# Optimization experiments

Measured on AMD Instinct MI355X. Metric: run time of the kernel, lower is better.

## Reference

```python
import jax, jax.numpy as jnp
import numpy as np

Q, M, B, D, H, DH, DI = 512, 512, 8, 1024, 16, 64, 4096
K = Q + M  # klen = rlen


def layer_norm(x, g, b, eps=1e-5):
    mu = x.mean(-1, keepdims=True)
    var = ((x - mu) ** 2).mean(-1, keepdims=True)
    return (x - mu) / jnp.sqrt(var + eps) * g + b


def rel_shift(x):
    # x: [qlen, klen, bsz, n_heads] -> Transformer-XL relative shift
    q, k = x.shape[0], x.shape[1]
    zero_pad = jnp.zeros((q, 1) + x.shape[2:], x.dtype)
    x_padded = jnp.concatenate([zero_pad, x], axis=1)          # [q, k+1, b, n]
    x_padded = x_padded.reshape((k + 1, q) + x.shape[2:])       # row-major reinterpret
    return x_padded[1:].reshape(x.shape)


def setup_inputs() -> dict:
    key = jax.random.key(0)
    ks = jax.random.split(key, 12)
    rn = lambda k, s: jax.random.normal(k, s, jnp.float32)
    # causal mask with memory: query i (absolute pos i+M) cannot attend to key j > i+M
    i = jnp.arange(Q)[:, None]
    j = jnp.arange(K)[None, :]
    attn_mask = (j > (i + M))[:, :, None]  # [Q, K, 1] bool
    return dict(
        w=rn(ks[0], (Q, B, D)),
        r=rn(ks[1], (K, D)),
        r_w_bias=rn(ks[2], (H, DH)) * 0.02,
        r_r_bias=rn(ks[3], (H, DH)) * 0.02,
        mems=rn(ks[4], (M, B, D)),
        attn_mask=attn_mask,
        Wqkv=rn(ks[5], (3 * H * DH, D)) * 0.02,
        Wr=rn(ks[6], (H * DH, D)) * 0.02,
        Wo=rn(ks[7], (D, H * DH)) * 0.02,
        ln1_g=jnp.ones(D), ln1_b=jnp.zeros(D),
        W1=rn(ks[8], (DI, D)) * 0.02, b1=jnp.zeros(DI),
        W2=rn(ks[9], (D, DI)) * 0.02, b2=jnp.zeros(D),
        ln2_g=jnp.ones(D), ln2_b=jnp.zeros(D),
    )


def reference(w, r, r_w_bias, r_r_bias, mems, attn_mask,
              Wqkv, Wr, Wo, ln1_g, ln1_b, W1, b1, W2, b2, ln2_g, ln2_b):
    qlen, bsz = w.shape[0], w.shape[1]
    scale = 1.0 / (DH ** 0.5)

    cat = jnp.concatenate([mems, w], axis=0)                 # [K, B, D]
    heads = cat @ Wqkv.T                                     # [K, B, 3*H*DH] (post-lnorm: no LN here)
    q, k, v = jnp.split(heads, 3, axis=-1)
    q = q[-qlen:]                                            # [Q, B, H*DH]
    r_k = r @ Wr.T                                           # [K, H*DH]

    klen = k.shape[0]
    q = q.reshape(qlen, bsz, H, DH)
    k = k.reshape(klen, bsz, H, DH)
    v = v.reshape(klen, bsz, H, DH)
    r_k = r_k.reshape(klen, H, DH)

    AC = jnp.einsum('ibnd,jbnd->ijbn', q + r_w_bias, k)      # content score
    BD = rel_shift(jnp.einsum('ibnd,jnd->ijbn', q + r_r_bias, r_k))  # position score
    attn_score = (AC + BD) * scale                           # [Q, K, B, H]
    attn_score = jnp.where(attn_mask[:, :, :, None], -jnp.inf, attn_score)

    attn_prob = jax.nn.softmax(attn_score, axis=1)
    attn_vec = jnp.einsum('ijbn,jbnd->ibnd', attn_prob, v)
    attn_vec = attn_vec.reshape(qlen, bsz, H * DH)
    attn_out = attn_vec @ Wo.T
    out1 = layer_norm(w + attn_out, ln1_g, ln1_b)            # post-lnorm residual

    ff = jax.nn.relu(out1 @ W1.T + b1) @ W2.T + b2           # position-wise FFN
    out = layer_norm(out1 + ff, ln2_g, ln2_b)
    return out
```

## Files before the change

kernel.cpp:

```cpp
#include <hip/hip_runtime.h>
#include <hip/hip_bf16.h>

typedef __hip_bfloat16 bf16;

typedef __attribute__((ext_vector_type(8))) short frag8;
typedef __attribute__((ext_vector_type(4))) float f32x4;

__device__ __forceinline__ bf16 f2bf(float f) { return __float2bfloat16(f); }

__device__ __forceinline__ float u16f(unsigned short u) {
  union { unsigned int i; float f; } c; c.i = ((unsigned int)u) << 16; return c.f;
}
__device__ __forceinline__ unsigned short bfbits(float f) {
  union { bf16 b; unsigned short u; } c; c.b = __float2bfloat16(f); return c.u;
}
__device__ __forceinline__ float tof(float x) { return x; }
__device__ __forceinline__ float tof(bf16 x)  { return __bfloat162float(x); }

__device__ __forceinline__ void gload_lds16(const bf16* g, short* l) {
  __builtin_amdgcn_global_load_lds(
      (const __attribute__((address_space(1))) void*)g,
      (__attribute__((address_space(3))) void*)l, 16, 0, 0);
}

template<int CTRL>
__device__ __forceinline__ float dppmax(float x) {
  return fmaxf(x, __int_as_float(__builtin_amdgcn_update_dpp(
      0, __float_as_int(x), CTRL, 0xF, 0xF, true)));
}
__device__ __forceinline__ float rowmax16(float x) {
  x = dppmax<0x128>(x);
  x = dppmax<0x124>(x);
  x = dppmax<0x4E>(x);
  x = dppmax<0xB1>(x);
  return x;
}
template<int CTRL>
__device__ __forceinline__ float dppadd(float x) {
  return x + __int_as_float(__builtin_amdgcn_update_dpp(
      0, __float_as_int(x), CTRL, 0xF, 0xF, true));
}
__device__ __forceinline__ float rowsum16(float x) {
  x = dppadd<0x128>(x);
  x = dppadd<0x124>(x);
  x = dppadd<0x4E>(x);
  x = dppadd<0xB1>(x);
  return x;
}

#define EP_PLAIN 0
#define EP_RK    2
#define EP_Q     3
#define EP_KV    4

struct CvtArgs {
  const float* src[8];
  bf16* dst[8];
  int cum[9];
};
__global__ __launch_bounds__(256)
void cvt8(CvtArgs a)
{
  const int i = blockIdx.x * 256 + threadIdx.x;
  if (i >= a.cum[8]) return;
  int seg = 7;
  #pragma unroll
  for (int s2 = 6; s2 >= 0; --s2) if (i < a.cum[s2 + 1]) seg = s2;
  const int o = i - a.cum[seg];
  float4 v = ((const float4*)a.src[seg])[o];
  ushort4 u;
  u.x = bfbits(v.x); u.y = bfbits(v.y); u.z = bfbits(v.z); u.w = bfbits(v.w);
  ((ushort4*)a.dst[seg])[o] = u;
}

template<typename TRES, int BKT>
__global__ __launch_bounds__(256)
void mgemm(const bf16* __restrict__ A, const bf16* __restrict__ W,
           const float* __restrict__ bias, const TRES* __restrict__ res,
           bf16* __restrict__ out,
           bf16* __restrict__ qwb, bf16* __restrict__ qrb,
           bf16* __restrict__ kbo, bf16* __restrict__ vto,
           const float* __restrict__ rwbias, const float* __restrict__ rrbias,
           int M, int N, int K, int mode, int relu, int gn, int CM, int CN)
{
  __shared__ __align__(16) short sAm[2][128 * BKT];
  __shared__ __align__(16) short sBm[2][128 * BKT];
  const int tid  = threadIdx.x;
  const int lane = tid & 63;
  const int wave = tid >> 6;
  const int quad = lane >> 4;
  const int l15  = lane & 15;
  const int xcd = blockIdx.x & 7;
  const int k_  = blockIdx.x >> 3;
  const int ncx = gn / CN;
  const int chy = xcd / ncx;
  const int chx = xcd - chy * ncx;
  const int m0 = (chy * CM + k_ / CN) * 128;
  const int n0 = (chx * CN + (k_ % CN)) * 128;
  const int wm = (wave >> 1) * 64;
  const int wn = (wave & 1) * 64;

  const int lr = tid >> 2;
  const int lc = (tid & 3) << 3;

  const bf16* aptr0 = A + (size_t)(m0 + lr) * K + lc;
  const bf16* aptr1 = aptr0 + (size_t)64 * K;
  const bf16* wptr0 = W + (size_t)(n0 + lr) * K + lc;
  const bf16* wptr1 = wptr0 + (size_t)64 * K;

  f32x4 acc[4][4] = {};

  auto stage = [&](int buf, int kk) {
    if constexpr (BKT == 32) {
      gload_lds16(aptr0 + kk, &sAm[buf][wave * 512]);
      gload_lds16(aptr1 + kk, &sAm[buf][2048 + wave * 512]);
      gload_lds16(wptr0 + kk, &sBm[buf][wave * 512]);
      gload_lds16(wptr1 + kk, &sBm[buf][2048 + wave * 512]);
    } else {
      #pragma unroll
      for (int p = 0; p < 4; ++p) {
        const int row = p * 32 + (tid >> 3);
        const int xb  = ((tid & 7) << 4) ^ ((row & 7) << 4);
        gload_lds16((const bf16*)((const char*)(A + (size_t)(m0 + row) * K + kk) + xb),
                    &sAm[buf][p * 2048 + wave * 512]);
        gload_lds16((const bf16*)((const char*)(W + (size_t)(n0 + row) * K + kk) + xb),
                    &sBm[buf][p * 2048 + wave * 512]);
      }
    }
  };

  stage(0, 0);
  __syncthreads();
  int cur = 0;

  for (int kk = 0; kk < K; kk += BKT) {
    if (kk + BKT < K) stage(cur ^ 1, kk + BKT);
    if constexpr (BKT == 32) {
      frag8 af[4], bfr[4];
      #pragma unroll
      for (int t = 0; t < 4; ++t) {
        af[t]  = *(const frag8*)&sAm[cur][(wm + t * 16 + l15) * 32 + quad * 8];
        bfr[t] = *(const frag8*)&sBm[cur][(wn + t * 16 + l15) * 32 + quad * 8];
      }
      #pragma unroll
      for (int mi = 0; mi < 4; ++mi)
        #pragma unroll
        for (int ni = 0; ni < 4; ++ni)
          acc[mi][ni] = __builtin_amdgcn_mfma_f32_16x16x32_bf16(
              af[mi], bfr[ni], acc[mi][ni], 0, 0, 0);
    } else {
      #pragma unroll
      for (int kf = 0; kf < 2; ++kf) {
        frag8 af[4], bfr[4];
        #pragma unroll
        for (int t = 0; t < 4; ++t) {
          const int ra = wm + t * 16 + l15;
          af[t] = *(const frag8*)((const char*)&sAm[cur][0] +
                    ra * 128 + ((kf * 64 + quad * 16) ^ ((ra & 7) << 4)));
          const int rb = wn + t * 16 + l15;
          bfr[t] = *(const frag8*)((const char*)&sBm[cur][0] +
                    rb * 128 + ((kf * 64 + quad * 16) ^ ((rb & 7) << 4)));
        }
        #pragma unroll
        for (int mi = 0; mi < 4; ++mi)
          #pragma unroll
          for (int ni = 0; ni < 4; ++ni)
            acc[mi][ni] = __builtin_amdgcn_mfma_f32_16x16x32_bf16(
                af[mi], bfr[ni], acc[mi][ni], 0, 0, 0);
      }
    }
    __syncthreads();
    cur ^= 1;
  }

  if (mode == EP_KV && n0 >= 1024) {
    short* smem = &sAm[0][0];
    #pragma unroll
    for (int mi = 0; mi < 4; ++mi) {
      #pragma unroll
      for (int reg = 0; reg < 4; ++reg) {
        const int rowl = wm + mi * 16 + quad * 4 + reg;
        const int bbl  = rowl & 7;
        const int tl   = rowl >> 3;
        #pragma unroll
        for (int ni = 0; ni < 4; ++ni) {
          const int coll = wn + ni * 16 + l15;
          const int hn2  = coll >> 6;
          const int d    = coll & 63;
          const int rowid = (bbl * 2 + hn2) * 64 + d;
          smem[tl * 1024 + (rowid ^ (tl << 1))] =
              (short)bfbits(acc[mi][ni][reg]);
        }
      }
    }
    __syncthreads();
    const int hnb = (n0 >> 6) - 16;
    const int t0  = m0 >> 3;
    #pragma unroll
    for (int p = 0; p < 4; ++p) {
      const int r   = p * 256 + tid;
      const int bbl = r >> 7;
      const int hn2 = (r >> 6) & 1;
      const int d   = r & 63;
      unsigned short tmp[16];
      #pragma unroll
      for (int tl = 0; tl < 16; ++tl)
        tmp[tl] = (unsigned short)smem[tl * 1024 + (r ^ (tl << 1))];
      bf16* dst = vto + ((size_t)(bbl * 16 + hnb + hn2) * 64 + d) * 1024 + t0;
      *(frag8*)dst       = *(const frag8*)&tmp[0];
      *(frag8*)(dst + 8) = *(const frag8*)&tmp[8];
    }
    return;
  }

  #pragma unroll
  for (int mi = 0; mi < 4; ++mi) {
    #pragma unroll
    for (int reg = 0; reg < 4; ++reg) {
      const int rowl = wm + mi * 16 + quad * 4 + reg;
      const int row  = m0 + rowl;
      if (mode == EP_PLAIN) {
        bf16* orow = out + (size_t)row * N;
        const TRES* rrow = res ? res + (size_t)row * N : nullptr;
        #pragma unroll
        for (int ni = 0; ni < 4; ++ni) {
          const int col = n0 + wn + ni * 16 + l15;
          float v = acc[mi][ni][reg];
          if (bias) v += bias[col];
          if (relu) v = fmaxf(v, 0.f);
          if (rrow) v += tof(rrow[col]);
          orow[col] = f2bf(v);
        }
      } else if (mode == EP_KV) {
        const int t = row >> 3, bb = row & 7;
        #pragma unroll
        for (int ni = 0; ni < 4; ++ni) {
          const int col = n0 + wn + ni * 16 + l15;
          const int hn = col >> 6, d = col & 63;
          kbo[((size_t)(bb * 16 + hn) * 1024 + t) * 64 + d] =
              f2bf(acc[mi][ni][reg]);
        }
      } else if (mode == EP_Q) {
        const int tq = row >> 3, bb = row & 7;
        #pragma unroll
        for (int ni = 0; ni < 4; ++ni) {
          const int col = n0 + wn + ni * 16 + l15;
          const int hn = col >> 6, d = col & 63;
          const float v = acc[mi][ni][reg];
          const size_t idx = ((size_t)(bb * 16 + hn) * 512 + tq) * 64 + d;
          qwb[idx] = f2bf(v + rwbias[col]);
          qrb[idx] = f2bf(v + rrbias[col]);
        }
      } else {
        #pragma unroll
        for (int ni = 0; ni < 4; ++ni) {
          const int col = n0 + wn + ni * 16 + l15;
          const int hn = col >> 6, d = col & 63;
          qwb[((size_t)hn * 1024 + row) * 64 + d] = f2bf(acc[mi][ni][reg]);
        }
      }
    }
  }
}

__global__ __launch_bounds__(256, 4)
void fattn(const bf16* __restrict__ qw, const bf16* __restrict__ qr,
           const bf16* __restrict__ kb, const bf16* __restrict__ vT,
           const bf16* __restrict__ rk, bf16* __restrict__ avec)
{
  __shared__ __align__(16) short sK[4096];
  __shared__ __align__(16) short sV[4096];
  __shared__ __align__(16) unsigned short p_lds[4][16][64];
  const int tid  = threadIdx.x;
  const int wave = tid >> 6, lane = tid & 63;
  const int quad = lane >> 4, l15 = lane & 15;
  const int bid = blockIdx.x;
  const int r_  = bid & 7;
  const int s_  = bid >> 3;
  const int phi = s_ & 15;
  const int it  = s_ >> 4;
  const int pr  = r_ + 8 * phi;
  const int h   = pr & 15;
  const int b   = pr >> 4;
  const int i0  = it * 64;
  const int iw  = i0 + wave * 16;
  const size_t bh = (size_t)b * 16 + h;
  const bf16* kp = kb + bh * 1024 * 64;
  const bf16* vp = vT + bh * 64 * 1024;
  const bf16* rp = rk + (size_t)h * 1024 * 64;

  frag8 aqw[2], aqr[2];
  {
    const bf16* r0 = qw + (bh * 512 + iw + l15) * 64 + quad * 8;
    aqw[0] = *(const frag8*)r0;
    aqw[1] = *(const frag8*)(r0 + 32);
    const bf16* r1 = qr + (bh * 512 + iw + l15) * 64 + quad * 8;
    aqr[0] = *(const frag8*)r1;
    aqr[1] = *(const frag8*)(r1 + 32);
  }

  f32x4 accO[4] = {};
  float m_run[4], l_run[4];
  #pragma unroll
  for (int rg = 0; rg < 4; ++rg) { m_run[rg] = -INFINITY; l_run[rg] = 0.f; }

  const int nsteps = ((i0 + 63 + 512) >> 6) + 1;
  const int offb   = 15 + l15 - quad * 4;

  auto stage = [&](int j0s) {
    #pragma unroll
    for (int c = 0; c < 2; ++c) {
      const int Lb = c * 4096 + tid * 16;
      const int r  = Lb >> 7;
      const int xb = (Lb & 127) ^ ((r & 7) << 4);
      short* dK = (short*)((char*)sK + (c * 4096 + wave * 1024));
      short* dV = (short*)((char*)sV + (c * 4096 + wave * 1024));
      gload_lds16((const bf16*)((const char*)kp + ((size_t)j0s + r) * 128 + xb), dK);
      gload_lds16((const bf16*)((const char*)vp + (size_t)r * 2048 + (size_t)j0s * 2 + xb), dV);
    }
  };
  stage(0);

  for (int jt = 0; jt < nsteps; ++jt) {
    const int j0 = jt << 6;
    const int pbase = 496 + j0 - iw;
    f32x4 bsub[5];
    #pragma unroll
    for (int ns = 0; ns < 5; ++ns) {
      const int prow = min(pbase + ns * 16 + l15, 1023);
      const bf16* rrow = rp + (size_t)prow * 64 + quad * 8;
      frag8 br0 = *(const frag8*)rrow;
      frag8 br1 = *(const frag8*)(rrow + 32);
      f32x4 z = {};
      z = __builtin_amdgcn_mfma_f32_16x16x32_bf16(aqr[0], br0, z, 0,0,0);
      bsub[ns] = __builtin_amdgcn_mfma_f32_16x16x32_bf16(aqr[1], br1, z, 0,0,0);
    }
    __syncthreads();
    f32x4 accS[4] = {};
    #pragma unroll
    for (int ns = 0; ns < 4; ++ns) {
      const int row = ns * 16 + l15;
      const int sw  = (row & 7) << 4;
      frag8 bk0 = *(const frag8*)((const char*)sK + ((row * 128 + quad * 16) ^ sw));
      frag8 bk1 = *(const frag8*)((const char*)sK + ((row * 128 + 64 + quad * 16) ^ sw));
      accS[ns] = __builtin_amdgcn_mfma_f32_16x16x32_bf16(aqw[0], bk0, accS[ns], 0,0,0);
      accS[ns] = __builtin_amdgcn_mfma_f32_16x16x32_bf16(aqw[1], bk1, accS[ns], 0,0,0);
    }
    float tmax[4];
    #pragma unroll
    for (int rg = 0; rg < 4; ++rg) {
      const int o    = offb - rg;
      const int srcl = (quad << 4) | (o & 15);
      const float s0 = __shfl(bsub[0][rg], srcl, 64);
      const float s1 = __shfl(bsub[1][rg], srcl, 64);
      const float s2 = __shfl(bsub[2][rg], srcl, 64);
      const float s3 = __shfl(bsub[3][rg], srcl, 64);
      const float s4 = __shfl(bsub[4][rg], srcl, 64);
      const bool hi  = (o & 16) != 0;
      const float bd0 = hi ? s1 : s0;
      const float bd1 = hi ? s2 : s1;
      const float bd2 = hi ? s3 : s2;
      const float bd3 = hi ? s4 : s3;
      const int jb   = j0 + l15;
      const int lim  = iw + quad * 4 + rg + 512;
      float v0 = (accS[0][rg] + bd0) * 0.125f;
      float v1 = (accS[1][rg] + bd1) * 0.125f;
      float v2 = (accS[2][rg] + bd2) * 0.125f;
      float v3 = (accS[3][rg] + bd3) * 0.125f;
      v0 = (jb      > lim) ? -INFINITY : v0;
      v1 = (jb + 16 > lim) ? -INFINITY : v1;
      v2 = (jb + 32 > lim) ? -INFINITY : v2;
      v3 = (jb + 48 > lim) ? -INFINITY : v3;
      accS[0][rg] = v0; accS[1][rg] = v1; accS[2][rg] = v2; accS[3][rg] = v3;
      tmax[rg] = rowmax16(fmaxf(fmaxf(v0, v1), fmaxf(v2, v3)));
    }
    float alpha[4], tsum[4] = {0.f, 0.f, 0.f, 0.f};
    #pragma unroll
    for (int rg = 0; rg < 4; ++rg) {
      const float nm = fmaxf(m_run[rg], tmax[rg]);
      alpha[rg] = __expf(m_run[rg] - nm);
      m_run[rg] = nm;
    }
    #pragma unroll
    for (int ns = 0; ns < 4; ++ns)
      #pragma unroll
      for (int rg = 0; rg < 4; ++rg) {
        const int rl = quad * 4 + rg;
        const float pv = __expf(accS[ns][rg] - m_run[rg]);
        tsum[rg] += pv;
        *(unsigned short*)((char*)&p_lds[wave][rl][0] +
            (((ns * 16 + l15) * 2) ^ ((rl & 7) << 4))) = bfbits(pv);
      }
    #pragma unroll
    for (int rg = 0; rg < 4; ++rg) {
      l_run[rg] = l_run[rg] * alpha[rg] + rowsum16(tsum[rg]);
      #pragma unroll
      for (int nd = 0; nd < 4; ++nd)
        accO[nd][rg] *= alpha[rg];
    }
    __builtin_amdgcn_wave_barrier();
    #pragma unroll
    for (int ks = 0; ks < 2; ++ks) {
      frag8 ap = *(const frag8*)((const char*)&p_lds[wave][l15][0] +
                  ((ks * 64 + quad * 16) ^ ((l15 & 7) << 4)));
      #pragma unroll
      for (int nd = 0; nd < 4; ++nd) {
        const int d = nd * 16 + l15;
        frag8 bv = *(const frag8*)((const char*)sV +
                    ((d * 128 + ks * 64 + quad * 16) ^ ((d & 7) << 4)));
        accO[nd] = __builtin_amdgcn_mfma_f32_16x16x32_bf16(ap, bv, accO[nd], 0,0,0);
      }
    }
    __builtin_amdgcn_wave_barrier();
    __syncthreads();
    if (jt + 1 < nsteps) stage((jt + 1) << 6);
  }

  #pragma unroll
  for (int rg = 0; rg < 4; ++rg) {
    const int i = iw + quad * 4 + rg;
    const float inv = 1.f / l_run[rg];
    #pragma unroll
    for (int nd = 0; nd < 4; ++nd) {
      const int d = nd * 16 + l15;
      avec[((size_t)i * 8 + b) * 1024 + h * 64 + d] = f2bf(accO[nd][rg] * inv);
    }
  }
}

template<typename TOUT>
__global__ __launch_bounds__(256)
void ln_kernel(const bf16* __restrict__ x, const float* __restrict__ g,
               const float* __restrict__ be, TOUT* __restrict__ out)
{
  __shared__ float red0[4];
  __shared__ float red1[4];
  const int row = blockIdx.x;
  const int tid = threadIdx.x;
  const bf16* xr = x + (size_t)row * 1024;
  ushort4 u = *(const ushort4*)(xr + (tid << 2));
  const float v0 = u16f(u.x), v1 = u16f(u.y), v2 = u16f(u.z), v3 = u16f(u.w);
  float sum = v0 + v1 + v2 + v3;
  #pragma unroll
  for (int off = 1; off < 64; off <<= 1) sum += __shfl_xor(sum, off, 64);
  if ((tid & 63) == 0) red0[tid >> 6] = sum;
  __syncthreads();
  const float mu = (red0[0] + red0[1] + red0[2] + red0[3]) * (1.f / 1024.f);
  const float d0 = v0 - mu, d1 = v1 - mu, d2 = v2 - mu, d3 = v3 - mu;
  float sq = d0*d0 + d1*d1 + d2*d2 + d3*d3;
  #pragma unroll
  for (int off = 1; off < 64; off <<= 1) sq += __shfl_xor(sq, off, 64);
  if ((tid & 63) == 0) red1[tid >> 6] = sq;
  __syncthreads();
  const float var = (red1[0] + red1[1] + red1[2] + red1[3]) * (1.f / 1024.f);
  const float inv = 1.f / sqrtf(var + 1e-5f);
  const int c = tid << 2;
  float4 ug = *(const float4*)(g + c);
  float4 ub = *(const float4*)(be + c);
  TOUT* orow = out + (size_t)row * 1024;
  orow[c+0] = (TOUT)(d0 * inv * ug.x + ub.x);
  orow[c+1] = (TOUT)(d1 * inv * ug.y + ub.y);
  orow[c+2] = (TOUT)(d2 * inv * ug.z + ub.z);
  orow[c+3] = (TOUT)(d3 * inv * ug.w + ub.w);
}

extern "C" void kernel_launch(void* const* d_in, const int* in_sizes, int n_in,
                              void* d_out, int out_size, void* d_ws, size_t ws_size,
                              hipStream_t stream)
{
  const float* w    = (const float*)d_in[0];
  const float* r    = (const float*)d_in[1];
  const float* rwb  = (const float*)d_in[2];
  const float* rrb  = (const float*)d_in[3];
  const float* mems = (const float*)d_in[4];
  const float* Wqkv = (const float*)d_in[6];
  const float* Wr   = (const float*)d_in[7];
  const float* Wo   = (const float*)d_in[8];
  const float* ln1g = (const float*)d_in[9];
  const float* ln1b = (const float*)d_in[10];
  const float* W1   = (const float*)d_in[11];
  const float* b1   = (const float*)d_in[12];
  const float* W2   = (const float*)d_in[13];
  const float* b2   = (const float*)d_in[14];
  const float* ln2g = (const float*)d_in[15];
  const float* ln2b = (const float*)d_in[16];

  const size_t MB = 1u << 20;
  char* p = (char*)d_ws;
  bf16* catb  = (bf16*)(p +  0 * MB);
  bf16* wqkvb = (bf16*)(p + 16 * MB);
  bf16* wrb   = (bf16*)(p + 22 * MB);
  bf16* wob   = (bf16*)(p + 24 * MB);
  bf16* w1b   = (bf16*)(p + 26 * MB);
  bf16* w2b   = (bf16*)(p + 34 * MB);
  bf16* qwbuf = (bf16*)(p + 42 * MB);
  bf16* qrbuf = (bf16*)(p + 50 * MB);
  bf16* kbuf  = (bf16*)(p + 58 * MB);
  bf16* vTbuf = (bf16*)(p + 74 * MB);
  bf16* rkbuf = (bf16*)(p + 90 * MB);
  bf16* rb    = (bf16*)(p + 92 * MB);
  bf16* avec  = (bf16*)(p +  0 * MB);
  bf16* x1    = (bf16*)(p +  8 * MB);
  bf16* o1    = (bf16*)(p + 42 * MB);
  bf16* x2    = (bf16*)(p + 50 * MB);
  bf16* h     = (bf16*)(p + 58 * MB);

  dim3 blk(256);
  {
    CvtArgs a;
    const int n4w = (4096 * 1024) / 4, n4r = (1024 * 1024) / 4,
              n4qkv = (3072 * 1024) / 4;
    a.src[0] = mems; a.dst[0] = catb;                        int n0_ = n4w;
    a.src[1] = w;    a.dst[1] = catb + (size_t)4096 * 1024;  int n1_ = n4w;
    a.src[2] = r;    a.dst[2] = rb;                          int n2_ = n4r;
    a.src[3] = Wqkv; a.dst[3] = wqkvb;                       int n3_ = n4qkv;
    a.src[4] = Wr;   a.dst[4] = wrb;                         int n4_ = n4r;
    a.src[5] = Wo;   a.dst[5] = wob;                         int n5_ = n4r;
    a.src[6] = W1;   a.dst[6] = w1b;                         int n6_ = n4w;
    a.src[7] = W2;   a.dst[7] = w2b;                         int n7_ = n4w;
    const int ns_[8] = {n0_, n1_, n2_, n3_, n4_, n5_, n6_, n7_};
    a.cum[0] = 0;
    for (int s2 = 0; s2 < 8; ++s2) a.cum[s2 + 1] = a.cum[s2] + ns_[s2];
    cvt8<<<dim3((a.cum[8] + 255) / 256), blk, 0, stream>>>(a);
  }

  mgemm<float, 32><<<dim3(1024), blk, 0, stream>>>(catb, wqkvb + (size_t)1024 * 1024,
        nullptr, (const float*)nullptr, nullptr, nullptr, nullptr, kbuf, vTbuf,
        nullptr, nullptr, 8192, 2048, 1024, EP_KV, 0, 16, 16, 8);
  mgemm<float, 64><<<dim3(256), blk, 0, stream>>>(catb + (size_t)4096 * 1024, wqkvb,
        nullptr, (const float*)nullptr, nullptr, qwbuf, qrbuf, nullptr, nullptr,
        rwb, rrb, 4096, 1024, 1024, EP_Q, 0, 8, 4, 8);
  mgemm<float, 64><<<dim3(64), blk, 0, stream>>>(rb, wrb, nullptr, (const float*)nullptr,
        nullptr, rkbuf, nullptr, nullptr, nullptr, nullptr, nullptr,
        1024, 1024, 1024, EP_RK, 0, 8, 2, 4);
  fattn<<<dim3(1024), blk, 0, stream>>>(qwbuf, qrbuf, kbuf, vTbuf, rkbuf, avec);
  mgemm<float, 64><<<dim3(256), blk, 0, stream>>>(avec, wob, nullptr, w,
        x1, nullptr, nullptr, nullptr, nullptr, nullptr, nullptr,
        4096, 1024, 1024, EP_PLAIN, 0, 8, 4, 8);
  ln_kernel<bf16><<<dim3(4096), blk, 0, stream>>>(x1, ln1g, ln1b, o1);
  mgemm<float, 32><<<dim3(1024), blk, 0, stream>>>(o1, w1b, b1, (const float*)nullptr,
        h, nullptr, nullptr, nullptr, nullptr, nullptr, nullptr,
        4096, 4096, 1024, EP_PLAIN, 1, 32, 8, 16);
  mgemm<bf16, 64><<<dim3(256), blk, 0, stream>>>(h, w2b, b2, o1,
        x2, nullptr, nullptr, nullptr, nullptr, nullptr, nullptr,
        4096, 1024, 4096, EP_PLAIN, 0, 8, 4, 8);
  ln_kernel<float><<<dim3(4096), blk, 0, stream>>>(x2, ln2g, ln2b, (float*)d_out);
}
```

Baseline: 536.1 us.

## Split-K the Wo and W2 GEMMs and fuse partial reduction into LayerNorm

```diff
diff --git a/kernel.cpp b/kernel.cpp
--- a/kernel.cpp
+++ b/kernel.cpp
@@ -52,6 +52,7 @@
 #define EP_RK    2
 #define EP_Q     3
 #define EP_KV    4
+#define EP_PART  5
 
 struct CvtArgs {
   const float* src[8];
@@ -77,11 +78,12 @@
 __global__ __launch_bounds__(256)
 void mgemm(const bf16* __restrict__ A, const bf16* __restrict__ W,
            const float* __restrict__ bias, const TRES* __restrict__ res,
-           bf16* __restrict__ out,
+           bf16* __restrict__ out, float* __restrict__ pout,
            bf16* __restrict__ qwb, bf16* __restrict__ qrb,
            bf16* __restrict__ kbo, bf16* __restrict__ vto,
            const float* __restrict__ rwbias, const float* __restrict__ rrbias,
-           int M, int N, int K, int mode, int relu, int gn, int CM, int CN)
+           int M, int N, int K, int Ks, int mode, int relu,
+           int gn, int CM, int CN, int sblk)
 {
   __shared__ __align__(16) short sAm[2][128 * BKT];
   __shared__ __align__(16) short sBm[2][128 * BKT];
@@ -90,8 +92,11 @@
   const int wave = tid >> 6;
   const int quad = lane >> 4;
   const int l15  = lane & 15;
-  const int xcd = blockIdx.x & 7;
-  const int k_  = blockIdx.x >> 3;
+  const int s     = blockIdx.x / sblk;
+  const int inner = blockIdx.x - s * sblk;
+  const int koff  = s * K;
+  const int xcd = inner & 7;
+  const int k_  = inner >> 3;
   const int ncx = gn / CN;
   const int chy = xcd / ncx;
   const int chx = xcd - chy * ncx;
@@ -103,10 +108,10 @@
   const int lr = tid >> 2;
   const int lc = (tid & 3) << 3;
 
-  const bf16* aptr0 = A + (size_t)(m0 + lr) * K + lc;
-  const bf16* aptr1 = aptr0 + (size_t)64 * K;
-  const bf16* wptr0 = W + (size_t)(n0 + lr) * K + lc;
-  const bf16* wptr1 = wptr0 + (size_t)64 * K;
+  const bf16* aptr0 = A + (size_t)(m0 + lr) * Ks + lc + koff;
+  const bf16* aptr1 = aptr0 + (size_t)64 * Ks;
+  const bf16* wptr0 = W + (size_t)(n0 + lr) * Ks + lc + koff;
+  const bf16* wptr1 = wptr0 + (size_t)64 * Ks;
 
   f32x4 acc[4][4] = {};
 
@@ -121,9 +126,9 @@
       for (int p = 0; p < 4; ++p) {
         const int row = p * 32 + (tid >> 3);
         const int xb  = ((tid & 7) << 4) ^ ((row & 7) << 4);
-        gload_lds16((const bf16*)((const char*)(A + (size_t)(m0 + row) * K + kk) + xb),
+        gload_lds16((const bf16*)((const char*)(A + (size_t)(m0 + row) * Ks + kk + koff) + xb),
                     &sAm[buf][p * 2048 + wave * 512]);
-        gload_lds16((const bf16*)((const char*)(W + (size_t)(n0 + row) * K + kk) + xb),
+        gload_lds16((const bf16*)((const char*)(W + (size_t)(n0 + row) * Ks + kk + koff) + xb),
                     &sBm[buf][p * 2048 + wave * 512]);
       }
     }
@@ -230,6 +235,13 @@
           if (relu) v = fmaxf(v, 0.f);
           if (rrow) v += tof(rrow[col]);
           orow[col] = f2bf(v);
+        }
+      } else if (mode == EP_PART) {
+        float* prow = pout + (size_t)s * M * N + (size_t)row * N;
+        #pragma unroll
+        for (int ni = 0; ni < 4; ++ni) {
+          const int col = n0 + wn + ni * 16 + l15;
+          prow[col] = acc[mi][ni][reg];
         }
       } else if (mode == EP_KV) {
         const int t = row >> 3, bb = row & 7;
@@ -464,6 +476,61 @@
   orow[c+3] = (TOUT)(d3 * inv * ug.w + ub.w);
 }
 
+template<typename TOUT, typename TRES>
+__global__ __launch_bounds__(256)
+void ln_red(const float* __restrict__ p0, const float* __restrict__ p1,
+            const TRES* __restrict__ res, const float* __restrict__ bias,
+            const float* __restrict__ g, const float* __restrict__ be,
+            TOUT* __restrict__ out)
+{
+  __shared__ float red0[4];
+  __shared__ float red1[4];
+  const int row = blockIdx.x;
+  const int tid = threadIdx.x;
+  const int c = tid << 2;
+  const size_t base = (size_t)row * 1024 + c;
+  float4 a0 = *(const float4*)(p0 + base);
+  float4 a1 = *(const float4*)(p1 + base);
+  float r0, r1, r2, r3;
+  if constexpr (sizeof(TRES) == 4) {
+    float4 rv = *(const float4*)((const float*)res + base);
+    r0 = rv.x; r1 = rv.y; r2 = rv.z; r3 = rv.w;
+  } else {
+    ushort4 u = *(const ushort4*)((const bf16*)res + base);
+    r0 = u16f(u.x); r1 = u16f(u.y); r2 = u16f(u.z); r3 = u16f(u.w);
+  }
+  float b0 = 0.f, b1 = 0.f, b2 = 0.f, b3 = 0.f;
+  if (bias) {
+    float4 bv = *(const float4*)(bias + c);
+    b0 = bv.x; b1 = bv.y; b2 = bv.z; b3 = bv.w;
+  }
+  const float v0 = r0 + a0.x + a1.x + b0;
+  const float v1 = r1 + a0.y + a1.y + b1;
+  const float v2 = r2 + a0.z + a1.z + b2;
+  const float v3 = r3 + a0.w + a1.w + b3;
+  float sum = v0 + v1 + v2 + v3;
+  #pragma unroll
+  for (int off = 1; off < 64; off <<= 1) sum += __shfl_xor(sum, off, 64);
+  if ((tid & 63) == 0) red0[tid >> 6] = sum;
+  __syncthreads();
+  const float mu = (red0[0] + red0[1] + red0[2] + red0[3]) * (1.f / 1024.f);
+  const float d0 = v0 - mu, d1 = v1 - mu, d2 = v2 - mu, d3 = v3 - mu;
+  float sq = d0*d0 + d1*d1 + d2*d2 + d3*d3;
+  #pragma unroll
+  for (int off = 1; off < 64; off <<= 1) sq += __shfl_xor(sq, off, 64);
+  if ((tid & 63) == 0) red1[tid >> 6] = sq;
+  __syncthreads();
+  const float var = (red1[0] + red1[1] + red1[2] + red1[3]) * (1.f / 1024.f);
+  const float inv = 1.f / sqrtf(var + 1e-5f);
+  float4 ug = *(const float4*)(g + c);
+  float4 ub = *(const float4*)(be + c);
+  TOUT* orow = out + (size_t)row * 1024;
+  orow[c+0] = (TOUT)(d0 * inv * ug.x + ub.x);
+  orow[c+1] = (TOUT)(d1 * inv * ug.y + ub.y);
+  orow[c+2] = (TOUT)(d2 * inv * ug.z + ub.z);
+  orow[c+3] = (TOUT)(d3 * inv * ug.w + ub.w);
+}
+
 extern "C" void kernel_launch(void* const* d_in, const int* in_sizes, int n_in,
                               void* d_out, int out_size, void* d_ws, size_t ws_size,
                               hipStream_t stream)
@@ -500,10 +567,10 @@
   bf16* rkbuf = (bf16*)(p + 90 * MB);
   bf16* rb    = (bf16*)(p + 92 * MB);
   bf16* avec  = (bf16*)(p +  0 * MB);
-  bf16* x1    = (bf16*)(p +  8 * MB);
   bf16* o1    = (bf16*)(p + 42 * MB);
-  bf16* x2    = (bf16*)(p + 50 * MB);
   bf16* h     = (bf16*)(p + 58 * MB);
+  float* woP  = (float*)(p + 58 * MB);
+  float* ffP  = (float*)(p +  0 * MB);
 
   dim3 blk(256);
   {
@@ -525,24 +592,26 @@
   }
 
   mgemm<float, 32><<<dim3(1024), blk, 0, stream>>>(catb, wqkvb + (size_t)1024 * 1024,
-        nullptr, (const float*)nullptr, nullptr, nullptr, nullptr, kbuf, vTbuf,
-        nullptr, nullptr, 8192, 2048, 1024, EP_KV, 0, 16, 16, 8);
+        nullptr, (const float*)nullptr, nullptr, nullptr, nullptr, nullptr, kbuf, vTbuf,
+        nullptr, nullptr, 8192, 2048, 1024, 1024, EP_KV, 0, 16, 16, 8, 1024);
   mgemm<float, 64><<<dim3(256), blk, 0, stream>>>(catb + (size_t)4096 * 1024, wqkvb,
-        nullptr, (const float*)nullptr, nullptr, qwbuf, qrbuf, nullptr, nullptr,
-        rwb, rrb, 4096, 1024, 1024, EP_Q, 0, 8, 4, 8);
+        nullptr, (const float*)nullptr, nullptr, nullptr, qwbuf, qrbuf, nullptr, nullptr,
+        rwb, rrb, 4096, 1024, 1024, 1024, EP_Q, 0, 8, 4, 8, 256);
   mgemm<float, 64><<<dim3(64), blk, 0, stream>>>(rb, wrb, nullptr, (const float*)nullptr,
-        nullptr, rkbuf, nullptr, nullptr, nullptr, nullptr, nullptr,
-        1024, 1024, 1024, EP_RK, 0, 8, 2, 4);
+        nullptr, nullptr, rkbuf, nullptr, nullptr, nullptr, nullptr, nullptr,
+        1024, 1024, 1024, 1024, EP_RK, 0, 8, 2, 4, 64);
   fattn<<<dim3(1024), blk, 0, stream>>>(qwbuf, qrbuf, kbuf, vTbuf, rkbuf, avec);
-  mgemm<float, 64><<<dim3(256), blk, 0, stream>>>(avec, wob, nullptr, w,
-        x1, nullptr, nullptr, nullptr, nullptr, nullptr, nullptr,
-        4096, 1024, 1024, EP_PLAIN, 0, 8, 4, 8);
-  ln_kernel<bf16><<<dim3(4096), blk, 0, stream>>>(x1, ln1g, ln1b, o1);
+  mgemm<float, 64><<<dim3(512), blk, 0, stream>>>(avec, wob, nullptr, (const float*)nullptr,
+        nullptr, woP, nullptr, nullptr, nullptr, nullptr, nullptr, nullptr,
+        4096, 1024, 512, 1024, EP_PART, 0, 8, 4, 8, 256);
+  ln_red<bf16, float><<<dim3(4096), blk, 0, stream>>>(
+        woP, woP + (size_t)4096 * 1024, w, nullptr, ln1g, ln1b, o1);
   mgemm<float, 32><<<dim3(1024), blk, 0, stream>>>(o1, w1b, b1, (const float*)nullptr,
-        h, nullptr, nullptr, nullptr, nullptr, nullptr, nullptr,
-        4096, 4096, 1024, EP_PLAIN, 1, 32, 8, 16);
-  mgemm<bf16, 64><<<dim3(256), blk, 0, stream>>>(h, w2b, b2, o1,
-        x2, nullptr, nullptr, nullptr, nullptr, nullptr, nullptr,
-        4096, 1024, 4096, EP_PLAIN, 0, 8, 4, 8);
-  ln_kernel<float><<<dim3(4096), blk, 0, stream>>>(x2, ln2g, ln2b, (float*)d_out);
-}
+        h, nullptr, nullptr, nullptr, nullptr, nullptr, nullptr, nullptr,
+        4096, 4096, 1024, 1024, EP_PLAIN, 1, 32, 8, 16, 1024);
+  mgemm<bf16, 64><<<dim3(512), blk, 0, stream>>>(h, w2b, nullptr, (const bf16*)nullptr,
+        nullptr, ffP, nullptr, nullptr, nullptr, nullptr, nullptr, nullptr,
+        4096, 1024, 2048, 4096, EP_PART, 0, 8, 4, 8, 256);
+  ln_red<float, bf16><<<dim3(4096), blk, 0, stream>>>(
+        ffP, ffP + (size_t)4096 * 1024, o1, b2, ln2g, ln2b, (float*)d_out);
+}
```

Result: faster. 491.0 us (-8.4%).
